# Kernel tuning notes

Hardware: AMD Instinct MI355X
Metric: run time of the kernel (lower is better)

## Reference

```python
import jax, jax.numpy as jnp
import numpy as np

NUM_HEADS = 8
NUM_LAYERS = 4
TOKEN_AMOUNT = 16
TOKEN_SIZE = 256
D_MODEL = 512
D_FF = 2048


def _layernorm(x, g, b, eps=1e-6):
    m = jnp.mean(x, axis=-1, keepdims=True)
    v = jnp.mean((x - m) ** 2, axis=-1, keepdims=True)
    return (x - m) / jnp.sqrt(v + eps) * g + b


def _mha(xq, xkv, W, b, mask, H):
    # W: [4, d, d] (q,k,v,o), b: [4, d]
    B, Tq, d = xq.shape
    Tk = xkv.shape[1]
    dh = d // H
    q = (xq @ W[0] + b[0]).reshape(B, Tq, H, dh).transpose(0, 2, 1, 3)
    k = (xkv @ W[1] + b[1]).reshape(B, Tk, H, dh).transpose(0, 2, 1, 3)
    v = (xkv @ W[2] + b[2]).reshape(B, Tk, H, dh).transpose(0, 2, 1, 3)
    logits = jnp.einsum('bhqd,bhkd->bhqk', q, k) / jnp.sqrt(jnp.float32(dh))
    if mask is not None:
        logits = logits - mask * jnp.finfo(jnp.float32).max
    w = jax.nn.softmax(logits, axis=-1)
    o = jnp.einsum('bhqk,bhkd->bhqd', w, v).transpose(0, 2, 1, 3).reshape(B, Tq, d)
    return o @ W[3] + b[3]


def _pos_enc(T, d):
    i = jnp.arange(d)
    factors = 1.0 / jnp.power(10000.0, (2.0 * (i // 2)).astype(jnp.float32) / d)
    ang = jnp.arange(T, dtype=jnp.float32)[:, None] * factors  # [T, d]
    return jnp.where(i % 2 == 0, jnp.sin(ang), jnp.cos(ang))


def setup_inputs() -> dict:
    key = jax.random.key(0)
    ks = jax.random.split(key, 8)
    B, Lenc, F = 16, 2048, 128
    d, dff, L, TS = D_MODEL, D_FF, NUM_LAYERS, TOKEN_SIZE
    s = 0.02
    return {
        'encoder_output': jax.random.normal(ks[0], (B, Lenc, d), jnp.float32),
        'encoder_input': jax.random.normal(ks[1], (B, Lenc, F), jnp.float32),
        'emb_W': jax.random.normal(ks[2], (TS, d), jnp.float32) * s,
        'emb_b': jnp.zeros((d,), jnp.float32),
        'out_W': jax.random.normal(ks[3], (d, TS), jnp.float32) * s,
        'out_b': jnp.zeros((TS,), jnp.float32),
        'self_W': jax.random.normal(ks[4], (L, 4, d, d), jnp.float32) * s,
        'self_b': jnp.zeros((L, 4, d), jnp.float32),
        'cross_W': jax.random.normal(ks[5], (L, 4, d, d), jnp.float32) * s,
        'cross_b': jnp.zeros((L, 4, d), jnp.float32),
        'ffn_W1': jax.random.normal(ks[6], (L, d, dff), jnp.float32) * s,
        'ffn_b1': jnp.zeros((L, dff), jnp.float32),
        'ffn_W2': jax.random.normal(ks[7], (L, dff, d), jnp.float32) * s,
        'ffn_b2': jnp.zeros((L, d), jnp.float32),
        'ln_g': jnp.ones((L, 3, d), jnp.float32),
        'ln_b': jnp.zeros((L, 3, d), jnp.float32),
    }


def reference(encoder_output, encoder_input, emb_W, emb_b, out_W, out_b,
              self_W, self_b, cross_W, cross_b,
              ffn_W1, ffn_b1, ffn_W2, ffn_b2, ln_g, ln_b):
    B = encoder_output.shape[0]
    d = emb_W.shape[1]
    H = NUM_HEADS
    # padding mask from encoder_input (mask_zero_inputs=True)
    pad_mask = jnp.min((encoder_input == 0).astype(jnp.float32), axis=2)[:, None, None, :]
    tokens = jnp.ones((B, 1, TOKEN_SIZE), dtype=jnp.float32)
    for _ in range(TOKEN_AMOUNT):
        T = tokens.shape[1]
        look_ahead = 1.0 - jnp.tril(jnp.ones((T, T), dtype=jnp.float32))
        tok_pad = jnp.min((tokens == 0).astype(jnp.float32), axis=2)[:, None, None, :]
        la_mask = jnp.maximum(tok_pad, look_ahead)
        x = (tokens @ emb_W + emb_b) * jnp.sqrt(jnp.float32(d)) + _pos_enc(T, d)
        for l in range(NUM_LAYERS):
            a = _mha(x, x, self_W[l], self_b[l], la_mask, H)
            x = _layernorm(x + a, ln_g[l, 0], ln_b[l, 0])
            c = _mha(x, encoder_output, cross_W[l], cross_b[l], pad_mask, H)
            x = _layernorm(x + c, ln_g[l, 1], ln_b[l, 1])
            f = jax.nn.relu(x @ ffn_W1[l] + ffn_b1[l]) @ ffn_W2[l] + ffn_b2[l]
            x = _layernorm(x + f, ln_g[l, 2], ln_b[l, 2])
        next_token = (x @ out_W + out_b)[:, -1:, :]
        tokens = jnp.concatenate([tokens, next_token], axis=1)
    return tokens[:, 1:, :]
```

## Files before the change

kernel.cpp:

```cpp
#include <hip/hip_runtime.h>


typedef unsigned short ushort_t;
typedef __attribute__((ext_vector_type(4))) float f32x4;
typedef __attribute__((ext_vector_type(8))) unsigned short us8;
typedef __attribute__((ext_vector_type(4))) unsigned short us4;

#define NB 256
#define NTHR 1024

__device__ __forceinline__ float bf2f(ushort_t u) {
    union { unsigned int i; float f; } v; v.i = ((unsigned int)u) << 16; return v.f;
}
__device__ __forceinline__ ushort_t f2bf(float f) {
    union { unsigned int i; float f; } v; v.f = f;
    return (ushort_t)((v.i + 0x7FFF + ((v.i >> 16) & 1)) >> 16);
}
__device__ __forceinline__ f32x4 b2f4(us4 w) {
    return (f32x4){bf2f(w[0]), bf2f(w[1]), bf2f(w[2]), bf2f(w[3])};
}
__device__ __forceinline__ float wave_sum(float v) {
    #pragma unroll
    for (int m = 32; m; m >>= 1) v += __shfl_xor(v, m);
    return v;
}
__device__ __forceinline__ float wave_max(float v) {
    #pragma unroll
    for (int m = 32; m; m >>= 1) v = fmaxf(v, __shfl_xor(v, m));
    return v;
}

union U64C { unsigned long long u; float2 f; us4 s4; };
__device__ __forceinline__ float clf(const float* p) {
    return __hip_atomic_load(p, __ATOMIC_RELAXED, __HIP_MEMORY_SCOPE_AGENT);
}
__device__ __forceinline__ void csf(float* p, float v) {
    __hip_atomic_store(p, v, __ATOMIC_RELAXED, __HIP_MEMORY_SCOPE_AGENT);
}
__device__ __forceinline__ float2 clf2(const float* p) {
    U64C c; c.u = __hip_atomic_load((unsigned long long*)p, __ATOMIC_RELAXED,
                                    __HIP_MEMORY_SCOPE_AGENT);
    return c.f;
}
__device__ __forceinline__ void csf2(float* p, float x, float y) {
    U64C c; c.f.x = x; c.f.y = y;
    __hip_atomic_store((unsigned long long*)p, c.u, __ATOMIC_RELAXED,
                       __HIP_MEMORY_SCOPE_AGENT);
}
__device__ __forceinline__ void csu4(ushort_t* p, us4 v) {
    U64C c; c.s4 = v;
    __hip_atomic_store((unsigned long long*)p, c.u, __ATOMIC_RELAXED,
                       __HIP_MEMORY_SCOPE_AGENT);
}

__device__ __forceinline__ void gbar(unsigned* bar, int g) {
    __syncthreads();
    if (threadIdx.x == 0) {
        unsigned* cnt = bar + g * 32;
        unsigned* rel = bar + 512 + g * 32;
        unsigned a = __hip_atomic_fetch_add(cnt, 1u, __ATOMIC_RELAXED,
                                            __HIP_MEMORY_SCOPE_AGENT);
        unsigned e = (a >> 4) + 1u;
        if ((a & 15u) == 15u) {
            __hip_atomic_store(rel, e, __ATOMIC_RELAXED, __HIP_MEMORY_SCOPE_AGENT);
        } else {
            while ((int)(__hip_atomic_load(rel, __ATOMIC_RELAXED,
                                           __HIP_MEMORY_SCOPE_AGENT) - e) < 0)
                __builtin_amdgcn_s_sleep(1);
        }
    }
    __syncthreads();
}

__device__ __forceinline__ void gbar_all(unsigned* bar) {
    __syncthreads();
    if (threadIdx.x == 0) {
        unsigned* cnt = bar + 1024;
        unsigned* rel = bar + 1056;
        unsigned a = __hip_atomic_fetch_add(cnt, 1u, __ATOMIC_RELAXED,
                                            __HIP_MEMORY_SCOPE_AGENT);
        unsigned e = (a >> 8) + 1u;
        if ((a & 255u) == 255u) {
            __hip_atomic_store(rel, e, __ATOMIC_RELAXED, __HIP_MEMORY_SCOPE_AGENT);
        } else {
            while ((int)(__hip_atomic_load(rel, __ATOMIC_RELAXED,
                                           __HIP_MEMORY_SCOPE_AGENT) - e) < 0)
                __builtin_amdgcn_s_sleep(1);
        }
    }
    __syncthreads();
}

__device__ __forceinline__ void ln512b(const float* __restrict__ row,
                                       const float* __restrict__ g,
                                       const float* __restrict__ be,
                                       int use_ln, float* dst, float* red) {
    int tid = threadIdx.x;
    float a = (tid < 512) ? clf(row + tid) : 0.f;
    if (use_ln) {
        float s = a, s2 = a * a;
        #pragma unroll
        for (int m = 32; m; m >>= 1) {
            s  += __shfl_xor(s, m);
            s2 += __shfl_xor(s2, m);
        }
        if ((tid & 63) == 0) { red[tid >> 6] = s; red[16 + (tid >> 6)] = s2; }
        __syncthreads();
        float ts = 0.f, ts2 = 0.f;
        #pragma unroll
        for (int i = 0; i < 8; i++) { ts += red[i]; ts2 += red[16 + i]; }
        float mu = ts * (1.f / 512.f);
        float var = ts2 * (1.f / 512.f) - mu * mu;
        float rstd = rsqrtf(var + 1e-6f);
        if (tid < 512) dst[tid] = (a - mu) * rstd * g[tid] + be[tid];
    } else {
        if (tid < 512) dst[tid] = a;
    }
    __syncthreads();
}

template<int NCQ, int K>
__device__ __forceinline__ void gemv_allf(const float* xs, const float* __restrict__ W,
                                          int ldw, int col0, float* part) {
    constexpr int S = 1024 / NCQ;
    constexpr int KS = K / S;
    int tid = threadIdx.x;
    int cq = tid & (NCQ - 1), ks = tid / NCQ;
    const float* Wp = W + (size_t)(ks * KS) * ldw + col0 + cq * 4;
    const float* xp = xs + ks * KS;
    f32x4 acc = {0.f, 0.f, 0.f, 0.f};
    #pragma unroll
    for (int r = 0; r < KS; r++)
        acc += xp[r] * *(const f32x4*)(Wp + (size_t)r * ldw);
    #pragma unroll
    for (int m = NCQ; m < 64; m <<= 1) {
        acc[0] += __shfl_xor(acc[0], m);
        acc[1] += __shfl_xor(acc[1], m);
        acc[2] += __shfl_xor(acc[2], m);
        acc[3] += __shfl_xor(acc[3], m);
    }
    int wave = tid >> 6, lane = tid & 63;
    if (lane < NCQ) *(f32x4*)(part + (wave * NCQ + lane) * 4) = acc;
    __syncthreads();
}

template<int NCQ, int K>
__device__ __forceinline__ void gemv_allb(const float* xs, const ushort_t* __restrict__ W,
                                          int ldw, int col0, float* part) {
    constexpr int S = 1024 / NCQ;
    constexpr int KS = K / S;
    int tid = threadIdx.x;
    int cq = tid & (NCQ - 1), ks = tid / NCQ;
    const ushort_t* Wp = W + (size_t)(ks * KS) * ldw + col0 + cq * 4;
    const float* xp = xs + ks * KS;
    f32x4 acc = {0.f, 0.f, 0.f, 0.f};
    #pragma unroll
    for (int r = 0; r < KS; r++)
        acc += xp[r] * b2f4(*(const us4*)(Wp + (size_t)r * ldw));
    #pragma unroll
    for (int m = NCQ; m < 64; m <<= 1) {
        acc[0] += __shfl_xor(acc[0], m);
        acc[1] += __shfl_xor(acc[1], m);
        acc[2] += __shfl_xor(acc[2], m);
        acc[3] += __shfl_xor(acc[3], m);
    }
    int wave = tid >> 6, lane = tid & 63;
    if (lane < NCQ) *(f32x4*)(part + (wave * NCQ + lane) * 4) = acc;
    __syncthreads();
}
template<int NCQ>
__device__ __forceinline__ float gemv_allr(const float* part) {
    float a = 0.f;
    #pragma unroll
    for (int w = 0; w < 16; w++) a += part[w * NCQ * 4 + threadIdx.x];
    return a;
}

struct Args {
    const float *enc, *encIn, *embW, *embB, *outW, *outB;
    const float *selfW, *selfB, *crossW, *crossB;
    const float *fW1, *fb1, *fW2, *fb2, *lng, *lnb;
    float* out;
    unsigned* bar;
    float *x0, *qbuf, *y1, *y2, *y3, *attnb;
    float *lny1, *lny2, *qt, *Pm2, *Ps2, *Pz, *tmpb, *selfK, *selfV;
    ushort_t *selfWb, *crossWb, *fW1b, *fW2b;
};


__global__ __launch_bounds__(NTHR, 4) void k_mega(Args A) {
    __shared__ ushort_t encL[128 * 520];
    __shared__ float padL[128];
    __shared__ float sm[6400];
    const int bid = blockIdx.x, tid = threadIdx.x;
    const int b = bid >> 4, r = bid & 15;
    unsigned* bar = A.bar;

    {
        const float* ep = A.enc + ((size_t)b * 2048 + r * 128) * 512;
        #pragma unroll 4
        for (int it = 0; it < 16; it++) {
            int idx = tid + it * 1024;
            int key = idx >> 7;
            int d = (idx & 127) * 4;
            float4 v = *(const float4*)(ep + (size_t)key * 512 + d);
            us4 o; o[0] = f2bf(v.x); o[1] = f2bf(v.y); o[2] = f2bf(v.z); o[3] = f2bf(v.w);
            *(us4*)(encL + key * 520 + d) = o;
        }
        int key = tid >> 3, sub = tid & 7;
        const float* p = A.encIn + ((size_t)b * 2048 + r * 128 + key) * 128 + sub * 16;
        int ok = 1;
        #pragma unroll
        for (int j = 0; j < 4; j++) {
            float4 v = *(const float4*)(p + j * 4);
            ok &= (v.x == 0.f) & (v.y == 0.f) & (v.z == 0.f) & (v.w == 0.f);
        }
        ok &= __shfl_xor(ok, 1); ok &= __shfl_xor(ok, 2); ok &= __shfl_xor(ok, 4);
        if (sub == 0) padL[key] = ok ? 1.f : 0.f;
        const float* srcs[4] = {A.selfW, A.crossW, A.fW1, A.fW2};
        ushort_t* dsts[4] = {A.selfWb, A.crossWb, A.fW1b, A.fW2b};
        #pragma unroll
        for (int a = 0; a < 4; a++) {
            const float* s = srcs[a];
            ushort_t* d = dsts[a];
            #pragma unroll
            for (int it = 0; it < 4; it++) {
                size_t i = (size_t)bid * 16384 + (size_t)(it * 1024 + tid) * 4;
                float4 v = *(const float4*)(s + i);
                us4 o; o[0] = f2bf(v.x); o[1] = f2bf(v.y); o[2] = f2bf(v.z); o[3] = f2bf(v.w);
                csu4(d + i, o);
            }
        }
    }
    gbar_all(bar);

    for (int t = 0; t < 16; t++) {
        {
            float* tok = sm;
            float* part = sm + 256;
            if (tid < 256)
                tok[tid] = (t == 0) ? 1.f
                         : clf(A.out + (size_t)b * 4096 + (t - 1) * 256 + tid);
            __syncthreads();
            gemv_allf<8, 256>(tok, A.embW, 512, r * 32, part);
            if (tid < 32) {
                float acc = gemv_allr<8>(part);
                int col = r * 32 + tid;
                float expo = (2.0f * (float)(col >> 1)) * (1.f / 512.f);
                float ang = (float)t * powf(10000.0f, -expo);
                float pv = (col & 1) ? cosf(ang) : sinf(ang);
                csf(A.x0 + (size_t)b * 512 + col,
                    (acc + A.embB[col]) * 22.627416997969522f + pv);
            }
        }
        gbar(bar, b);

        for (int l = 0; l < 4; l++) {
            const float* src = (l == 0) ? A.x0 : A.y3;
            const float* gP = (l == 0) ? nullptr : A.lng + ((l - 1) * 3 + 2) * 512;
            const float* bP = (l == 0) ? nullptr : A.lnb + ((l - 1) * 3 + 2) * 512;
            int ulnP = (l != 0);

            {
                float* xs = sm;
                float* red = sm + 512;
                float* part = sm + 1024;
                ln512b(src + (size_t)b * 512, gP, bP, ulnP, xs, red);
                int cq = tid & 7, ks = tid >> 3;
                const float* xp = xs + ks * 4;
                f32x4 a0 = {0.f,0.f,0.f,0.f}, a1 = a0, a2 = a0;
                const ushort_t* W0 = A.selfWb + ((size_t)(l * 4 + 0)) * 262144
                                   + (size_t)(ks * 4) * 512 + r * 32 + cq * 4;
                const ushort_t* W1 = W0 + 262144;
                const ushort_t* W2 = W1 + 262144;
                #pragma unroll
                for (int rr = 0; rr < 4; rr++) {
                    float x = xp[rr];
                    a0 += x * b2f4(*(const us4*)(W0 + (size_t)rr * 512));
                    a1 += x * b2f4(*(const us4*)(W1 + (size_t)rr * 512));
                    a2 += x * b2f4(*(const us4*)(W2 + (size_t)rr * 512));
                }
                #pragma unroll
                for (int m = 8; m < 64; m <<= 1) {
                    #pragma unroll
                    for (int j = 0; j < 4; j++) {
                        a0[j] += __shfl_xor(a0[j], m);
                        a1[j] += __shfl_xor(a1[j], m);
                        a2[j] += __shfl_xor(a2[j], m);
                    }
                }
                int wave = tid >> 6, lane = tid & 63;
                if (lane < 8) {
                    *(f32x4*)(part + (wave * 8 + lane) * 4) = a0;
                    *(f32x4*)(part + 512 + (wave * 8 + lane) * 4) = a1;
                    *(f32x4*)(part + 1024 + (wave * 8 + lane) * 4) = a2;
                }
                __syncthreads();
                if (tid < 96) {
                    int m = tid >> 5, j = tid & 31;
                    float a = 0.f;
                    #pragma unroll
                    for (int w = 0; w < 16; w++) a += part[m * 512 + w * 32 + j];
                    int col = r * 32 + j;
                    a += A.selfB[(l * 4 + m) * 512 + col];
                    if (m == 0) csf(A.qbuf + (size_t)b * 512 + col, a);
                    else if (m == 1)
                        csf(A.selfK + (((size_t)l * 16 + b) * 16 + t) * 512 + col, a);
                    else
                        csf(A.selfV + (((size_t)l * 16 + b) * 16 + t) * 512 + col, a);
                }
            }
            gbar(bar, b);

            {
                float* xr = sm;
                float* qs = sm + 512;
                float* as2 = sm + 1024;
                float* lg = sm + 2048;
                float* red = sm + 2176;
                float* part = sm + 2560;
                ln512b(src + (size_t)b * 512, gP, bP, ulnP, xr, red);
                if (tid < 256) {
                    float2 v = clf2(A.qbuf + (size_t)b * 512 + tid * 2);
                    qs[tid * 2] = v.x; qs[tid * 2 + 1] = v.y;
                }
                __syncthreads();
                const float* Kb = A.selfK + ((size_t)l * 16 + b) * 16 * 512;
                const float* Vb = A.selfV + ((size_t)l * 16 + b) * 16 * 512;
                if (tid < 512) {
                    int idx = tid >> 2, q4 = tid & 3;
                    int h = idx >> 4, j = idx & 15;
                    if (j <= t) {
                        const float* kp = Kb + (size_t)j * 512 + h * 64 + q4 * 16;
                        const float* qp = qs + h * 64 + q4 * 16;
                        float s = 0.f;
                        #pragma unroll
                        for (int d = 0; d < 16; d += 2) {
                            float2 kv = clf2(kp + d);
                            s += qp[d] * kv.x + qp[d + 1] * kv.y;
                        }
                        s += __shfl_xor(s, 1);
                        s += __shfl_xor(s, 2);
                        if (q4 == 0) lg[h * 16 + j] = s * 0.125f;
                    }
                }
                __syncthreads();
                if (tid < 8) {
                    float m = -1e30f;
                    for (int j = 0; j <= t; j++) m = fmaxf(m, lg[tid * 16 + j]);
                    float ssum = 0.f;
                    for (int j = 0; j <= t; j++) {
                        float e = __expf(lg[tid * 16 + j] - m);
                        lg[tid * 16 + j] = e; ssum += e;
                    }
                    float inv = 1.f / ssum;
                    for (int j = 0; j <= t; j++) lg[tid * 16 + j] *= inv;
                }
                __syncthreads();
                {
                    int col = tid & 511, jh = tid >> 9;
                    float a = 0.f;
                    for (int j = jh; j <= t; j += 2)
                        a += lg[(col >> 6) * 16 + j] * clf(Vb + (size_t)j * 512 + col);
                    as2[jh * 512 + col] = a;
                }
                __syncthreads();
                if (tid < 512) qs[tid] = as2[tid] + as2[512 + tid];
                __syncthreads();
                gemv_allb<8, 512>(qs, A.selfWb + ((size_t)(l * 4 + 3)) * 262144,
                                  512, r * 32, part);
                if (tid < 32) {
                    int col = r * 32 + tid;
                    csf(A.y1 + (size_t)b * 512 + col,
                        gemv_allr<8>(part) + A.selfB[(l * 4 + 3) * 512 + col] + xr[col]);
                }
            }
            gbar(bar, b);

            {
                int h = r >> 1, half = r & 1;
                float* xsw = sm;
                float* red = sm + 512;
                float* qch = sm + 544;
                float* part = sm + 1024;
                ln512b(A.y1 + (size_t)b * 512, A.lng + (l * 3) * 512,
                       A.lnb + (l * 3) * 512, 1, xsw, red);
                if (r == 0 && tid < 512)
                    csf(A.lny1 + (size_t)b * 512 + tid, xsw[tid]);
                gemv_allb<16, 512>(xsw, A.crossWb + ((size_t)(l * 4)) * 262144,
                                   512, h * 64, part);
                if (tid < 64)
                    qch[tid] = gemv_allr<16>(part)
                             + A.crossB[(l * 4) * 512 + h * 64 + tid];
                __syncthreads();
                {
                    int D = half * 256 + (tid >> 2), q4 = tid & 3;
                    const ushort_t* wr = A.crossWb + ((size_t)(l * 4 + 1)) * 262144
                                       + (size_t)D * 512 + h * 64 + q4 * 16;
                    const float* qp = qch + q4 * 16;
                    float a = 0.f;
                    #pragma unroll
                    for (int j = 0; j < 16; j += 4) {
                        f32x4 wv = b2f4(*(const us4*)(wr + j));
                        a += qp[j]*wv[0] + qp[j+1]*wv[1] + qp[j+2]*wv[2] + qp[j+3]*wv[3];
                    }
                    a += __shfl_xor(a, 1);
                    a += __shfl_xor(a, 2);
                    if (q4 == 0)
                        csf(A.qt + ((size_t)b * 8 + h) * 512 + D, a * 0.125f);
                }
            }
            gbar(bar, b);

            {
                float* qts = sm;
                float* lge = sm + 4160;
                float* wms = sm + 5184;
                float* wss = sm + 5200;
                #pragma unroll
                for (int it = 0; it < 2; it++) {
                    int p = (tid + it * 1024) * 2;
                    float2 v = clf2(A.qt + (size_t)b * 4096 + p);
                    int row = p >> 9, d = p & 511;
                    qts[row * 520 + d] = v.x;
                    qts[row * 520 + d + 1] = v.y;
                }
                __syncthreads();
                #pragma unroll
                for (int it = 0; it < 4; it++) {
                    int key = it * 32 + (tid >> 5);
                    int hh = (tid >> 2) & 7, pq = tid & 3;
                    const ushort_t* er = encL + key * 520;
                    const float* q = qts + hh * 520;
                    float a0 = 0.f, a1 = 0.f;
                    #pragma unroll
                    for (int ch = 0; ch < 16; ch++) {
                        int c8 = (pq + ch * 4) * 8;
                        us8 ev8 = *(const us8*)(er + c8);
                        const float* qp = q + c8;
                        a0 += bf2f(ev8[0])*qp[0] + bf2f(ev8[1])*qp[1]
                            + bf2f(ev8[2])*qp[2] + bf2f(ev8[3])*qp[3];
                        a1 += bf2f(ev8[4])*qp[4] + bf2f(ev8[5])*qp[5]
                            + bf2f(ev8[6])*qp[6] + bf2f(ev8[7])*qp[7];
                    }
                    float acc = a0 + a1;
                    acc += __shfl_xor(acc, 1);
                    acc += __shfl_xor(acc, 2);
                    if (pq == 0)
                        lge[hh * 128 + key] = (padL[key] != 0.f) ? -2e30f : acc;
                }
                __syncthreads();
                {
                    int hh = tid >> 7, k = tid & 127;
                    float lv = lge[hh * 128 + k];
                    float mv = wave_max(lv);
                    if ((tid & 63) == 0) wms[tid >> 6] = mv;
                    __syncthreads();
                    float m = fmaxf(wms[hh * 2], wms[hh * 2 + 1]);
                    float ev = __expf(lv - m);
                    float sv = wave_sum(ev);
                    if ((tid & 63) == 0) wss[tid >> 6] = sv;
                    lge[hh * 128 + k] = ev;
                    __syncthreads();
                    if (tid < 8) {
                        int bc = b * 16 + r;
                        csf(A.Pm2 + bc * 8 + tid, fmaxf(wms[tid * 2], wms[tid * 2 + 1]));
                        csf(A.Ps2 + bc * 8 + tid, wss[tid * 2] + wss[tid * 2 + 1]);
                    }
                }
                __syncthreads();
                {
                    int hz = tid >> 7, ii = tid & 127;
                    f32x4 z = {0.f, 0.f, 0.f, 0.f};
                    const ushort_t* ep2 = encL + ii * 4;
                    const float* le = lge + hz * 128;
                    #pragma unroll 4
                    for (int k = 0; k < 128; k++) {
                        float ev = le[k];
                        us4 e4 = *(const us4*)(ep2 + k * 520);
                        z[0] += ev * bf2f(e4[0]); z[1] += ev * bf2f(e4[1]);
                        z[2] += ev * bf2f(e4[2]); z[3] += ev * bf2f(e4[3]);
                    }
                    float* dst = A.Pz + ((size_t)((b * 16 + r) * 8 + hz)) * 512 + ii * 4;
                    csf2(dst, z[0], z[1]);
                    csf2(dst + 2, z[2], z[3]);
                }
            }
            gbar(bar, b);

            {
                int h = r >> 1, half = r & 1;
                float* zs = sm;
                float* zs2 = sm + 512;
                float* ecs = sm + 2560;
                float* part = sm + 2624;
                if (tid < 16) {
                    float mcv = clf(A.Pm2 + (b * 16 + tid) * 8 + h);
                    float mm = mcv;
                    mm = fmaxf(mm, __shfl_xor(mm, 1));
                    mm = fmaxf(mm, __shfl_xor(mm, 2));
                    mm = fmaxf(mm, __shfl_xor(mm, 4));
                    mm = fmaxf(mm, __shfl_xor(mm, 8));
                    float ec = __expf(mcv - mm);
                    float sv = ec * clf(A.Ps2 + (b * 16 + tid) * 8 + h);
                    sv += __shfl_xor(sv, 1); sv += __shfl_xor(sv, 2);
                    sv += __shfl_xor(sv, 4); sv += __shfl_xor(sv, 8);
                    ecs[tid] = ec;
                    if (tid == 0) ecs[16] = 1.f / sv;
                }
                __syncthreads();
                {
                    int cp = (tid & 255) * 2, qtr = tid >> 8;
                    float a0 = 0.f, a1 = 0.f;
                    #pragma unroll
                    for (int j = 0; j < 4; j++) {
                        int cc = qtr * 4 + j;
                        float2 v = clf2(A.Pz + ((size_t)(b * 16 + cc) * 8 + h) * 512 + cp);
                        a0 += ecs[cc] * v.x; a1 += ecs[cc] * v.y;
                    }
                    zs2[qtr * 512 + cp] = a0;
                    zs2[qtr * 512 + cp + 1] = a1;
                }
                __syncthreads();
                if (tid < 512)
                    zs[tid] = (zs2[tid] + zs2[512 + tid] + zs2[1024 + tid]
                             + zs2[1536 + tid]) * ecs[16];
                __syncthreads();
                gemv_allb<8, 512>(zs, A.crossWb + ((size_t)(l * 4 + 2)) * 262144,
                                  512, h * 64 + half * 32, part);
                if (tid < 32) {
                    int col = h * 64 + half * 32 + tid;
                    csf(A.attnb + (size_t)b * 512 + col,
                        gemv_allr<8>(part) + A.crossB[(l * 4 + 2) * 512 + col]);
                }
            }
            gbar(bar, b);

            {
                float* xa = sm;
                float* part = sm + 512;
                if (tid < 256) {
                    float2 v = clf2(A.attnb + (size_t)b * 512 + tid * 2);
                    xa[tid * 2] = v.x; xa[tid * 2 + 1] = v.y;
                }
                __syncthreads();
                gemv_allb<8, 512>(xa, A.crossWb + ((size_t)(l * 4 + 3)) * 262144,
                                  512, r * 32, part);
                if (tid < 32) {
                    int col = r * 32 + tid;
                    csf(A.y2 + (size_t)b * 512 + col,
                        gemv_allr<8>(part) + A.crossB[(l * 4 + 3) * 512 + col]
                        + clf(A.lny1 + (size_t)b * 512 + col));
                }
            }
            gbar(bar, b);

            {
                float* xsw = sm;
                float* red = sm + 512;
                float* part = sm + 1024;
                ln512b(A.y2 + (size_t)b * 512, A.lng + (l * 3 + 1) * 512,
                       A.lnb + (l * 3 + 1) * 512, 1, xsw, red);
                if (r == 0 && tid < 512)
                    csf(A.lny2 + (size_t)b * 512 + tid, xsw[tid]);
                gemv_allb<32, 512>(xsw, A.fW1b + (size_t)l * 512 * 2048,
                                   2048, r * 128, part);
                if (tid < 128) {
                    int col = r * 128 + tid;
                    csf(A.tmpb + (size_t)b * 2048 + col,
                        fmaxf(gemv_allr<32>(part) + A.fb1[l * 2048 + col], 0.f));
                }
            }
            gbar(bar, b);

            {
                float* ts = sm;
                float* part = sm + 2048;
                {
                    float2 v = clf2(A.tmpb + (size_t)b * 2048 + tid * 2);
                    ts[tid * 2] = v.x; ts[tid * 2 + 1] = v.y;
                }
                __syncthreads();
                gemv_allb<8, 2048>(ts, A.fW2b + (size_t)l * 2048 * 512,
                                   512, r * 32, part);
                if (tid < 32) {
                    int col = r * 32 + tid;
                    csf(A.y3 + (size_t)b * 512 + col,
                        gemv_allr<8>(part) + A.fb2[l * 512 + col]
                        + clf(A.lny2 + (size_t)b * 512 + col));
                }
            }
            gbar(bar, b);
        }

        {
            float* xsw = sm;
            float* red = sm + 512;
            float* part = sm + 1024;
            ln512b(A.y3 + (size_t)b * 512, A.lng + 11 * 512, A.lnb + 11 * 512,
                   1, xsw, red);
            gemv_allf<4, 512>(xsw, A.outW, 256, r * 16, part);
            if (tid < 16) {
                int col = r * 16 + tid;
                csf(A.out + (size_t)b * 4096 + t * 256 + col,
                    gemv_allr<4>(part) + A.outB[col]);
            }
        }
        gbar(bar, b);
    }
}


extern "C" void kernel_launch(void* const* d_in, const int* in_sizes, int n_in,
                              void* d_out, int out_size, void* d_ws, size_t ws_size,
                              hipStream_t stream) {
    Args A;
    A.enc    = (const float*)d_in[0];
    A.encIn  = (const float*)d_in[1];
    A.embW   = (const float*)d_in[2];
    A.embB   = (const float*)d_in[3];
    A.outW   = (const float*)d_in[4];
    A.outB   = (const float*)d_in[5];
    A.selfW  = (const float*)d_in[6];
    A.selfB  = (const float*)d_in[7];
    A.crossW = (const float*)d_in[8];
    A.crossB = (const float*)d_in[9];
    A.fW1    = (const float*)d_in[10];
    A.fb1    = (const float*)d_in[11];
    A.fW2    = (const float*)d_in[12];
    A.fb2    = (const float*)d_in[13];
    A.lng    = (const float*)d_in[14];
    A.lnb    = (const float*)d_in[15];
    A.out    = (float*)d_out;

    char* ws = (char*)d_ws;
    size_t off = 0;
    auto alloc = [&](size_t bytes) -> char* {
        char* p = ws + off;
        off = (off + bytes + 255) & ~(size_t)255;
        return p;
    };
    char* barrier = alloc(8192);
    A.bar = (unsigned*)barrier;
    A.x0    = (float*)alloc(16 * 512 * 4);
    A.qbuf  = (float*)alloc(16 * 512 * 4);
    A.y1    = (float*)alloc(16 * 512 * 4);
    A.y2    = (float*)alloc(16 * 512 * 4);
    A.y3    = (float*)alloc(16 * 512 * 4);
    A.attnb = (float*)alloc(16 * 512 * 4);
    A.lny1  = (float*)alloc(16 * 512 * 4);
    A.lny2  = (float*)alloc(16 * 512 * 4);
    A.qt    = (float*)alloc((size_t)16 * 8 * 512 * 4);
    A.Pm2   = (float*)alloc(16 * 16 * 8 * 4);
    A.Ps2   = (float*)alloc(16 * 16 * 8 * 4);
    A.Pz    = (float*)alloc((size_t)16 * 16 * 8 * 512 * 4);
    A.tmpb  = (float*)alloc((size_t)16 * 2048 * 4);
    A.selfK = (float*)alloc((size_t)4 * 16 * 16 * 512 * 4);
    A.selfV = (float*)alloc((size_t)4 * 16 * 16 * 512 * 4);
    A.selfWb  = (ushort_t*)alloc((size_t)4 * 4 * 512 * 512 * 2);
    A.crossWb = (ushort_t*)alloc((size_t)4 * 4 * 512 * 512 * 2);
    A.fW1b    = (ushort_t*)alloc((size_t)4 * 512 * 2048 * 2);
    A.fW2b    = (ushort_t*)alloc((size_t)4 * 2048 * 512 * 2);
    if (off > ws_size) return;

    hipMemsetAsync(barrier, 0, 8192, stream);
    k_mega<<<dim3(NB), dim3(NTHR), 0, stream>>>(A);
}
```

Baseline: 4.860 ms.

## Compute output projection and embedding redundantly per block to drop grid barriers

Each block now computes the full output-logit projection and the next-token embedding locally from bf16 copies of the output and embedding weights. This removes the per-token x0 round trip and two group barriers per decode step; the loop runs one extra iteration to emit the final token. Self-attention score and value-weighted sums are also re-parallelised across all 1024 threads with vector loads. The cost is 16x redundant work on these small GEMVs, plus bf16 rounding of the embedding and output weights, which changes numerics.

```diff
diff --git a/kernel.cpp b/kernel.cpp
--- a/kernel.cpp
+++ b/kernel.cpp
@@ -71,7 +71,6 @@
     }
     __syncthreads();
 }
-
 __device__ __forceinline__ void gbar_all(unsigned* bar) {
     __syncthreads();
     if (threadIdx.x == 0) {
@@ -94,53 +93,24 @@
 __device__ __forceinline__ void ln512b(const float* __restrict__ row,
                                        const float* __restrict__ g,
                                        const float* __restrict__ be,
-                                       int use_ln, float* dst, float* red) {
+                                       float* dst, float* red) {
     int tid = threadIdx.x;
     float a = (tid < 512) ? clf(row + tid) : 0.f;
-    if (use_ln) {
-        float s = a, s2 = a * a;
-        #pragma unroll
-        for (int m = 32; m; m >>= 1) {
-            s  += __shfl_xor(s, m);
-            s2 += __shfl_xor(s2, m);
-        }
-        if ((tid & 63) == 0) { red[tid >> 6] = s; red[16 + (tid >> 6)] = s2; }
-        __syncthreads();
-        float ts = 0.f, ts2 = 0.f;
-        #pragma unroll
-        for (int i = 0; i < 8; i++) { ts += red[i]; ts2 += red[16 + i]; }
-        float mu = ts * (1.f / 512.f);
-        float var = ts2 * (1.f / 512.f) - mu * mu;
-        float rstd = rsqrtf(var + 1e-6f);
-        if (tid < 512) dst[tid] = (a - mu) * rstd * g[tid] + be[tid];
-    } else {
-        if (tid < 512) dst[tid] = a;
+    float s = a, s2 = a * a;
+    #pragma unroll
+    for (int m = 32; m; m >>= 1) {
+        s  += __shfl_xor(s, m);
+        s2 += __shfl_xor(s2, m);
     }
+    if ((tid & 63) == 0) { red[tid >> 6] = s; red[16 + (tid >> 6)] = s2; }
     __syncthreads();
-}
-
-template<int NCQ, int K>
-__device__ __forceinline__ void gemv_allf(const float* xs, const float* __restrict__ W,
-                                          int ldw, int col0, float* part) {
-    constexpr int S = 1024 / NCQ;
-    constexpr int KS = K / S;
-    int tid = threadIdx.x;
-    int cq = tid & (NCQ - 1), ks = tid / NCQ;
-    const float* Wp = W + (size_t)(ks * KS) * ldw + col0 + cq * 4;
-    const float* xp = xs + ks * KS;
-    f32x4 acc = {0.f, 0.f, 0.f, 0.f};
+    float ts = 0.f, ts2 = 0.f;
     #pragma unroll
-    for (int r = 0; r < KS; r++)
-        acc += xp[r] * *(const f32x4*)(Wp + (size_t)r * ldw);
-    #pragma unroll
-    for (int m = NCQ; m < 64; m <<= 1) {
-        acc[0] += __shfl_xor(acc[0], m);
-        acc[1] += __shfl_xor(acc[1], m);
-        acc[2] += __shfl_xor(acc[2], m);
-        acc[3] += __shfl_xor(acc[3], m);
-    }
-    int wave = tid >> 6, lane = tid & 63;
-    if (lane < NCQ) *(f32x4*)(part + (wave * NCQ + lane) * 4) = acc;
+    for (int i = 0; i < 8; i++) { ts += red[i]; ts2 += red[16 + i]; }
+    float mu = ts * (1.f / 512.f);
+    float var = ts2 * (1.f / 512.f) - mu * mu;
+    float rstd = rsqrtf(var + 1e-6f);
+    if (tid < 512) dst[tid] = (a - mu) * rstd * g[tid] + be[tid];
     __syncthreads();
 }
 
@@ -182,9 +152,9 @@
     const float *fW1, *fb1, *fW2, *fb2, *lng, *lnb;
     float* out;
     unsigned* bar;
-    float *x0, *qbuf, *y1, *y2, *y3, *attnb;
+    float *qbuf, *y1, *y2, *y3, *attnb;
     float *lny1, *lny2, *qt, *Pm2, *Ps2, *Pz, *tmpb, *selfK, *selfV;
-    ushort_t *selfWb, *crossWb, *fW1b, *fW2b;
+    ushort_t *selfWb, *crossWb, *fW1b, *fW2b, *embWb, *outWb;
 };
 
 
@@ -231,41 +201,92 @@
                 csu4(d + i, o);
             }
         }
+        if (bid < 8) {
+            #pragma unroll
+            for (int it = 0; it < 4; it++) {
+                size_t i = (size_t)bid * 16384 + (size_t)(it * 1024 + tid) * 4;
+                float4 v = *(const float4*)(A.embW + i);
+                us4 o; o[0] = f2bf(v.x); o[1] = f2bf(v.y); o[2] = f2bf(v.z); o[3] = f2bf(v.w);
+                csu4(A.embWb + i, o);
+            }
+        } else if (bid < 16) {
+            #pragma unroll
+            for (int it = 0; it < 4; it++) {
+                size_t i = (size_t)(bid - 8) * 16384 + (size_t)(it * 1024 + tid) * 4;
+                float4 v = *(const float4*)(A.outW + i);
+                us4 o; o[0] = f2bf(v.x); o[1] = f2bf(v.y); o[2] = f2bf(v.z); o[3] = f2bf(v.w);
+                csu4(A.outWb + i, o);
+            }
+        }
     }
     gbar_all(bar);
 
-    for (int t = 0; t < 16; t++) {
+    for (int t = 0; t < 17; t++) {
         {
-            float* tok = sm;
-            float* part = sm + 256;
-            if (tid < 256)
-                tok[tid] = (t == 0) ? 1.f
-                         : clf(A.out + (size_t)b * 4096 + (t - 1) * 256 + tid);
-            __syncthreads();
-            gemv_allf<8, 256>(tok, A.embW, 512, r * 32, part);
-            if (tid < 32) {
-                float acc = gemv_allr<8>(part);
-                int col = r * 32 + tid;
-                float expo = (2.0f * (float)(col >> 1)) * (1.f / 512.f);
-                float ang = (float)t * powf(10000.0f, -expo);
-                float pv = (col & 1) ? cosf(ang) : sinf(ang);
-                csf(A.x0 + (size_t)b * 512 + col,
-                    (acc + A.embB[col]) * 22.627416997969522f + pv);
-            }
-        }
-        gbar(bar, b);
+            float* xs = sm;
+            float* red = sm + 512;
+            float* tokb = sm + 544;
+            float* part = sm + 1024;
+            if (t == 0) {
+                if (tid < 256) tokb[tid] = 1.f;
+                __syncthreads();
+            } else {
+                ln512b(A.y3 + (size_t)b * 512, A.lng + 11 * 512, A.lnb + 11 * 512,
+                       xs, red);
+                int cq = tid & 63, ks = tid >> 6;
+                const ushort_t* Wp = A.outWb + (size_t)(ks * 32) * 256 + cq * 4;
+                const float* xp = xs + ks * 32;
+                f32x4 acc = {0.f, 0.f, 0.f, 0.f};
+                #pragma unroll
+                for (int k = 0; k < 32; k++)
+                    acc += xp[k] * b2f4(*(const us4*)(Wp + (size_t)k * 256));
+                *(f32x4*)(part + ks * 256 + cq * 4) = acc;
+                __syncthreads();
+                if (tid < 256) {
+                    float a = 0.f;
+                    #pragma unroll
+                    for (int s = 0; s < 16; s++) a += part[s * 256 + tid];
+                    a += A.outB[tid];
+                    tokb[tid] = a;
+                    if ((tid >> 4) == r)
+                        A.out[(size_t)b * 4096 + (t - 1) * 256 + tid] = a;
+                }
+                __syncthreads();
+            }
+            if (t == 16) break;
+            {
+                int cq = tid & 127, ks = tid >> 7;
+                const ushort_t* Wp = A.embWb + (size_t)(ks * 32) * 512 + cq * 4;
+                const float* xp = tokb + ks * 32;
+                f32x4 acc = {0.f, 0.f, 0.f, 0.f};
+                #pragma unroll
+                for (int k = 0; k < 32; k++)
+                    acc += xp[k] * b2f4(*(const us4*)(Wp + (size_t)k * 512));
+                *(f32x4*)(part + ks * 512 + cq * 4) = acc;
+                __syncthreads();
+                if (tid < 512) {
+                    float a = 0.f;
+                    #pragma unroll
+                    for (int s = 0; s < 8; s++) a += part[s * 512 + tid];
+                    float expo = (2.0f * (float)(tid >> 1)) * (1.f / 512.f);
+                    float ang = (float)t * powf(10000.0f, -expo);
+                    float pv = (tid & 1) ? cosf(ang) : sinf(ang);
+                    xs[tid] = (a + A.embB[tid]) * 22.627416997969522f + pv;
+                }
+                __syncthreads();
+            }
+        }
 
         for (int l = 0; l < 4; l++) {
-            const float* src = (l == 0) ? A.x0 : A.y3;
-            const float* gP = (l == 0) ? nullptr : A.lng + ((l - 1) * 3 + 2) * 512;
-            const float* bP = (l == 0) ? nullptr : A.lnb + ((l - 1) * 3 + 2) * 512;
-            int ulnP = (l != 0);
+            const float* src = A.y3;
+            const float* gP = A.lng + ((l - 1) * 3 + 2) * 512;
+            const float* bP = A.lnb + ((l - 1) * 3 + 2) * 512;
 
             {
                 float* xs = sm;
                 float* red = sm + 512;
                 float* part = sm + 1024;
-                ln512b(src + (size_t)b * 512, gP, bP, ulnP, xs, red);
+                if (l) ln512b(src + (size_t)b * 512, gP, bP, xs, red);
                 int cq = tid & 7, ks = tid >> 3;
                 const float* xp = xs + ks * 4;
                 f32x4 a0 = {0.f,0.f,0.f,0.f}, a1 = a0, a2 = a0;
@@ -316,10 +337,10 @@
                 float* xr = sm;
                 float* qs = sm + 512;
                 float* as2 = sm + 1024;
-                float* lg = sm + 2048;
-                float* red = sm + 2176;
-                float* part = sm + 2560;
-                ln512b(src + (size_t)b * 512, gP, bP, ulnP, xr, red);
+                float* lg = sm + 5120;
+                float* red = sm + 5248;
+                float* part = sm + 5280;
+                if (l) ln512b(src + (size_t)b * 512, gP, bP, xr, red);
                 if (tid < 256) {
                     float2 v = clf2(A.qbuf + (size_t)b * 512 + tid * 2);
                     qs[tid * 2] = v.x; qs[tid * 2 + 1] = v.y;
@@ -327,21 +348,20 @@
                 __syncthreads();
                 const float* Kb = A.selfK + ((size_t)l * 16 + b) * 16 * 512;
                 const float* Vb = A.selfV + ((size_t)l * 16 + b) * 16 * 512;
-                if (tid < 512) {
-                    int idx = tid >> 2, q4 = tid & 3;
+                {
+                    int idx = tid >> 3, kp = tid & 7;
                     int h = idx >> 4, j = idx & 15;
                     if (j <= t) {
-                        const float* kp = Kb + (size_t)j * 512 + h * 64 + q4 * 16;
-                        const float* qp = qs + h * 64 + q4 * 16;
-                        float s = 0.f;
-                        #pragma unroll
-                        for (int d = 0; d < 16; d += 2) {
-                            float2 kv = clf2(kp + d);
-                            s += qp[d] * kv.x + qp[d + 1] * kv.y;
-                        }
+                        const float* kpp = Kb + (size_t)j * 512 + h * 64 + kp * 8;
+                        const float* qp = qs + h * 64 + kp * 8;
+                        float4 k0 = *(const float4*)kpp;
+                        float4 k1 = *(const float4*)(kpp + 4);
+                        float s = qp[0]*k0.x + qp[1]*k0.y + qp[2]*k0.z + qp[3]*k0.w
+                                + qp[4]*k1.x + qp[5]*k1.y + qp[6]*k1.z + qp[7]*k1.w;
                         s += __shfl_xor(s, 1);
                         s += __shfl_xor(s, 2);
-                        if (q4 == 0) lg[h * 16 + j] = s * 0.125f;
+                        s += __shfl_xor(s, 4);
+                        if (kp == 0) lg[h * 16 + j] = s * 0.125f;
                     }
                 }
                 __syncthreads();
@@ -358,14 +378,24 @@
                 }
                 __syncthreads();
                 {
-                    int col = tid & 511, jh = tid >> 9;
+                    int cq2 = tid & 127, js = tid >> 7;
+                    int col0 = cq2 * 4, h = col0 >> 6;
+                    f32x4 acc = {0.f, 0.f, 0.f, 0.f};
+                    for (int j = js; j <= t; j += 8) {
+                        float4 v = *(const float4*)(Vb + (size_t)j * 512 + col0);
+                        float w = lg[h * 16 + j];
+                        acc[0] += w * v.x; acc[1] += w * v.y;
+                        acc[2] += w * v.z; acc[3] += w * v.w;
+                    }
+                    *(f32x4*)(as2 + js * 512 + col0) = acc;
+                }
+                __syncthreads();
+                if (tid < 512) {
                     float a = 0.f;
-                    for (int j = jh; j <= t; j += 2)
-                        a += lg[(col >> 6) * 16 + j] * clf(Vb + (size_t)j * 512 + col);
-                    as2[jh * 512 + col] = a;
-                }
-                __syncthreads();
-                if (tid < 512) qs[tid] = as2[tid] + as2[512 + tid];
+                    #pragma unroll
+                    for (int s = 0; s < 8; s++) a += as2[s * 512 + tid];
+                    qs[tid] = a;
+                }
                 __syncthreads();
                 gemv_allb<8, 512>(qs, A.selfWb + ((size_t)(l * 4 + 3)) * 262144,
                                   512, r * 32, part);
@@ -384,7 +414,7 @@
                 float* qch = sm + 544;
                 float* part = sm + 1024;
                 ln512b(A.y1 + (size_t)b * 512, A.lng + (l * 3) * 512,
-                       A.lnb + (l * 3) * 512, 1, xsw, red);
+                       A.lnb + (l * 3) * 512, xsw, red);
                 if (r == 0 && tid < 512)
                     csf(A.lny1 + (size_t)b * 512 + tid, xsw[tid]);
                 gemv_allb<16, 512>(xsw, A.crossWb + ((size_t)(l * 4)) * 262144,
@@ -560,7 +590,7 @@
                 float* red = sm + 512;
                 float* part = sm + 1024;
                 ln512b(A.y2 + (size_t)b * 512, A.lng + (l * 3 + 1) * 512,
-                       A.lnb + (l * 3 + 1) * 512, 1, xsw, red);
+                       A.lnb + (l * 3 + 1) * 512, xsw, red);
                 if (r == 0 && tid < 512)
                     csf(A.lny2 + (size_t)b * 512 + tid, xsw[tid]);
                 gemv_allb<32, 512>(xsw, A.fW1b + (size_t)l * 512 * 2048,
@@ -592,21 +622,6 @@
             }
             gbar(bar, b);
         }
-
-        {
-            float* xsw = sm;
-            float* red = sm + 512;
-            float* part = sm + 1024;
-            ln512b(A.y3 + (size_t)b * 512, A.lng + 11 * 512, A.lnb + 11 * 512,
-                   1, xsw, red);
-            gemv_allf<4, 512>(xsw, A.outW, 256, r * 16, part);
-            if (tid < 16) {
-                int col = r * 16 + tid;
-                csf(A.out + (size_t)b * 4096 + t * 256 + col,
-                    gemv_allr<4>(part) + A.outB[col]);
-            }
-        }
-        gbar(bar, b);
     }
 }
 
@@ -642,7 +657,6 @@
     };
     char* barrier = alloc(8192);
     A.bar = (unsigned*)barrier;
-    A.x0    = (float*)alloc(16 * 512 * 4);
     A.qbuf  = (float*)alloc(16 * 512 * 4);
     A.y1    = (float*)alloc(16 * 512 * 4);
     A.y2    = (float*)alloc(16 * 512 * 4);
@@ -661,6 +675,8 @@
     A.crossWb = (ushort_t*)alloc((size_t)4 * 4 * 512 * 512 * 2);
     A.fW1b    = (ushort_t*)alloc((size_t)4 * 512 * 2048 * 2);
     A.fW2b    = (ushort_t*)alloc((size_t)4 * 2048 * 512 * 2);
+    A.embWb   = (ushort_t*)alloc((size_t)256 * 512 * 2);
+    A.outWb   = (ushort_t*)alloc((size_t)512 * 256 * 2);
     if (off > ws_size) return;
 
     hipMemsetAsync(barrier, 0, 8192, stream);
```

New measurement: 5.281 ms. +8.6%, slower.

## Compute full QKV redundantly per block to drop a group barrier

Applied to the files above, without the earlier changes.

Each of the 16 blocks serving a batch row now computes the full Q, K and V projections for the current token in shared memory, instead of one column slice each. This removes the qbuf round-trip through global memory and one group barrier per layer per token. The current token's K/V come from shared memory, while older positions are read from the global K/V cache. The attention score and value accumulation are also re-partitioned across all threads. The cost is 16x redundant weight reads and multiply-adds for the QKV projections across the blocks of each batch row.

```diff
diff --git a/kernel.cpp b/kernel.cpp
--- a/kernel.cpp
+++ b/kernel.cpp
@@ -71,7 +71,6 @@
     }
     __syncthreads();
 }
-
 __device__ __forceinline__ void gbar_all(unsigned* bar) {
     __syncthreads();
     if (threadIdx.x == 0) {
@@ -182,7 +181,7 @@
     const float *fW1, *fb1, *fW2, *fb2, *lng, *lnb;
     float* out;
     unsigned* bar;
-    float *x0, *qbuf, *y1, *y2, *y3, *attnb;
+    float *x0, *y1, *y2, *y3, *attnb;
     float *lny1, *lny2, *qt, *Pm2, *Ps2, *Pz, *tmpb, *selfK, *selfV;
     ushort_t *selfWb, *crossWb, *fW1b, *fW2b;
 };
@@ -262,86 +261,66 @@
             int ulnP = (l != 0);
 
             {
-                float* xs = sm;
+                float* xs  = sm;
                 float* red = sm + 512;
-                float* part = sm + 1024;
+                float* qf  = sm + 544;
+                float* kf  = sm + 1056;
+                float* vf  = sm + 1568;
+                float* lg  = sm + 2080;
+                float* part= sm + 2304;
                 ln512b(src + (size_t)b * 512, gP, bP, ulnP, xs, red);
-                int cq = tid & 7, ks = tid >> 3;
-                const float* xp = xs + ks * 4;
-                f32x4 a0 = {0.f,0.f,0.f,0.f}, a1 = a0, a2 = a0;
-                const ushort_t* W0 = A.selfWb + ((size_t)(l * 4 + 0)) * 262144
-                                   + (size_t)(ks * 4) * 512 + r * 32 + cq * 4;
-                const ushort_t* W1 = W0 + 262144;
-                const ushort_t* W2 = W1 + 262144;
-                #pragma unroll
-                for (int rr = 0; rr < 4; rr++) {
-                    float x = xp[rr];
-                    a0 += x * b2f4(*(const us4*)(W0 + (size_t)rr * 512));
-                    a1 += x * b2f4(*(const us4*)(W1 + (size_t)rr * 512));
-                    a2 += x * b2f4(*(const us4*)(W2 + (size_t)rr * 512));
-                }
-                #pragma unroll
-                for (int m = 8; m < 64; m <<= 1) {
-                    #pragma unroll
-                    for (int j = 0; j < 4; j++) {
-                        a0[j] += __shfl_xor(a0[j], m);
-                        a1[j] += __shfl_xor(a1[j], m);
-                        a2[j] += __shfl_xor(a2[j], m);
-                    }
-                }
-                int wave = tid >> 6, lane = tid & 63;
-                if (lane < 8) {
-                    *(f32x4*)(part + (wave * 8 + lane) * 4) = a0;
-                    *(f32x4*)(part + 512 + (wave * 8 + lane) * 4) = a1;
-                    *(f32x4*)(part + 1024 + (wave * 8 + lane) * 4) = a2;
-                }
-                __syncthreads();
-                if (tid < 96) {
-                    int m = tid >> 5, j = tid & 31;
-                    float a = 0.f;
-                    #pragma unroll
-                    for (int w = 0; w < 16; w++) a += part[m * 512 + w * 32 + j];
-                    int col = r * 32 + j;
-                    a += A.selfB[(l * 4 + m) * 512 + col];
-                    if (m == 0) csf(A.qbuf + (size_t)b * 512 + col, a);
-                    else if (m == 1)
-                        csf(A.selfK + (((size_t)l * 16 + b) * 16 + t) * 512 + col, a);
-                    else
-                        csf(A.selfV + (((size_t)l * 16 + b) * 16 + t) * 512 + col, a);
-                }
-            }
-            gbar(bar, b);
-
-            {
-                float* xr = sm;
-                float* qs = sm + 512;
-                float* as2 = sm + 1024;
-                float* lg = sm + 2048;
-                float* red = sm + 2176;
-                float* part = sm + 2560;
-                ln512b(src + (size_t)b * 512, gP, bP, ulnP, xr, red);
-                if (tid < 256) {
-                    float2 v = clf2(A.qbuf + (size_t)b * 512 + tid * 2);
-                    qs[tid * 2] = v.x; qs[tid * 2 + 1] = v.y;
-                }
-                __syncthreads();
+                auto fullgemv = [&](const ushort_t* W, const float* bias, float* dst) {
+                    int cq = tid & 127, ks = tid >> 7;
+                    const ushort_t* Wp = W + (size_t)(ks * 64) * 512 + cq * 4;
+                    const float* xp = xs + ks * 64;
+                    f32x4 acc = {0.f, 0.f, 0.f, 0.f};
+                    #pragma unroll 8
+                    for (int rr = 0; rr < 64; rr++)
+                        acc += xp[rr] * b2f4(*(const us4*)(Wp + (size_t)rr * 512));
+                    *(f32x4*)(part + ks * 512 + cq * 4) = acc;
+                    __syncthreads();
+                    if (tid < 512) {
+                        float a = 0.f;
+                        #pragma unroll
+                        for (int s = 0; s < 8; s++) a += part[s * 512 + tid];
+                        dst[tid] = a + bias[tid];
+                    }
+                    __syncthreads();
+                };
+                fullgemv(A.selfWb + ((size_t)(l * 4 + 0)) * 262144,
+                         A.selfB + (l * 4 + 0) * 512, qf);
+                fullgemv(A.selfWb + ((size_t)(l * 4 + 1)) * 262144,
+                         A.selfB + (l * 4 + 1) * 512, kf);
+                fullgemv(A.selfWb + ((size_t)(l * 4 + 2)) * 262144,
+                         A.selfB + (l * 4 + 2) * 512, vf);
+                if (tid < 32) {
+                    int col = r * 32 + tid;
+                    csf(A.selfK + (((size_t)l * 16 + b) * 16 + t) * 512 + col, kf[col]);
+                    csf(A.selfV + (((size_t)l * 16 + b) * 16 + t) * 512 + col, vf[col]);
+                }
                 const float* Kb = A.selfK + ((size_t)l * 16 + b) * 16 * 512;
                 const float* Vb = A.selfV + ((size_t)l * 16 + b) * 16 * 512;
-                if (tid < 512) {
-                    int idx = tid >> 2, q4 = tid & 3;
+                {
+                    int idx = tid >> 3, kp = tid & 7;
                     int h = idx >> 4, j = idx & 15;
                     if (j <= t) {
-                        const float* kp = Kb + (size_t)j * 512 + h * 64 + q4 * 16;
-                        const float* qp = qs + h * 64 + q4 * 16;
-                        float s = 0.f;
-                        #pragma unroll
-                        for (int d = 0; d < 16; d += 2) {
-                            float2 kv = clf2(kp + d);
-                            s += qp[d] * kv.x + qp[d + 1] * kv.y;
+                        const float* qp = qf + h * 64 + kp * 8;
+                        float s;
+                        if (j == t) {
+                            const float* kpp = kf + h * 64 + kp * 8;
+                            s = qp[0]*kpp[0] + qp[1]*kpp[1] + qp[2]*kpp[2] + qp[3]*kpp[3]
+                              + qp[4]*kpp[4] + qp[5]*kpp[5] + qp[6]*kpp[6] + qp[7]*kpp[7];
+                        } else {
+                            const float* kpp = Kb + (size_t)j * 512 + h * 64 + kp * 8;
+                            float4 k0 = *(const float4*)kpp;
+                            float4 k1 = *(const float4*)(kpp + 4);
+                            s = qp[0]*k0.x + qp[1]*k0.y + qp[2]*k0.z + qp[3]*k0.w
+                              + qp[4]*k1.x + qp[5]*k1.y + qp[6]*k1.z + qp[7]*k1.w;
                         }
                         s += __shfl_xor(s, 1);
                         s += __shfl_xor(s, 2);
-                        if (q4 == 0) lg[h * 16 + j] = s * 0.125f;
+                        s += __shfl_xor(s, 4);
+                        if (kp == 0) lg[h * 16 + j] = s * 0.125f;
                     }
                 }
                 __syncthreads();
@@ -358,21 +337,37 @@
                 }
                 __syncthreads();
                 {
-                    int col = tid & 511, jh = tid >> 9;
+                    int cq2 = tid & 127, js = tid >> 7;
+                    int col0 = cq2 * 4, h = col0 >> 6;
+                    f32x4 acc = {0.f, 0.f, 0.f, 0.f};
+                    for (int j = js; j <= t; j += 8) {
+                        float w = lg[h * 16 + j];
+                        if (j == t) {
+                            const float* vp = vf + col0;
+                            acc[0] += w * vp[0]; acc[1] += w * vp[1];
+                            acc[2] += w * vp[2]; acc[3] += w * vp[3];
+                        } else {
+                            float4 v = *(const float4*)(Vb + (size_t)j * 512 + col0);
+                            acc[0] += w * v.x; acc[1] += w * v.y;
+                            acc[2] += w * v.z; acc[3] += w * v.w;
+                        }
+                    }
+                    *(f32x4*)(part + js * 512 + col0) = acc;
+                }
+                __syncthreads();
+                if (tid < 512) {
                     float a = 0.f;
-                    for (int j = jh; j <= t; j += 2)
-                        a += lg[(col >> 6) * 16 + j] * clf(Vb + (size_t)j * 512 + col);
-                    as2[jh * 512 + col] = a;
-                }
-                __syncthreads();
-                if (tid < 512) qs[tid] = as2[tid] + as2[512 + tid];
-                __syncthreads();
-                gemv_allb<8, 512>(qs, A.selfWb + ((size_t)(l * 4 + 3)) * 262144,
+                    #pragma unroll
+                    for (int s = 0; s < 8; s++) a += part[s * 512 + tid];
+                    qf[tid] = a;
+                }
+                __syncthreads();
+                gemv_allb<8, 512>(qf, A.selfWb + ((size_t)(l * 4 + 3)) * 262144,
                                   512, r * 32, part);
                 if (tid < 32) {
                     int col = r * 32 + tid;
                     csf(A.y1 + (size_t)b * 512 + col,
-                        gemv_allr<8>(part) + A.selfB[(l * 4 + 3) * 512 + col] + xr[col]);
+                        gemv_allr<8>(part) + A.selfB[(l * 4 + 3) * 512 + col] + xs[col]);
                 }
             }
             gbar(bar, b);
@@ -643,7 +638,6 @@
     char* barrier = alloc(8192);
     A.bar = (unsigned*)barrier;
     A.x0    = (float*)alloc(16 * 512 * 4);
-    A.qbuf  = (float*)alloc(16 * 512 * 4);
     A.y1    = (float*)alloc(16 * 512 * 4);
     A.y2    = (float*)alloc(16 * 512 * 4);
     A.y3    = (float*)alloc(16 * 512 * 4);
```

Result: slower. 7.660 ms (+57.6%).
